# Performance work log

Hardware: AMD Instinct MI355X
Metric: run time of the kernel (lower is better)

## Reference

```python
import jax, jax.numpy as jnp
import numpy as np

N, D = 8192, 128
NUM_CLASSES = 512
LA, UA, K, S, LAMBDA_G, MARGIN = 10.0, 110.0, 3.0, 30.0, 1.0, 0.0


def setup_inputs() -> dict:
    key = jax.random.key(0)
    k1, k2, k3 = jax.random.split(key, 3)
    feat = jax.random.normal(k1, (N, D), dtype=jnp.float32)
    uc = jax.random.uniform(k2, (N,), dtype=jnp.float32)
    label = jax.random.randint(k3, (N,), 0, NUM_CLASSES, dtype=jnp.int64)
    return {"feat": feat, "uc": uc, "label": label}


def _safe_sqrt(d2):
    # matches torch cdist subgradient: grad 0 at exactly-zero distance
    pos = d2 > 0
    return jnp.where(pos, jnp.sqrt(jnp.where(pos, d2, 1.0)), 0.0)


def reference(feat, uc, label):
    # --- norm regularizer g (reg_type='exp_3') ---
    norms = jnp.linalg.norm(feat, axis=-1)                      # [N]
    nx = (norms - LA) / (UA - LA)
    ug = 2.7183 ** (-K)
    reg = ((jnp.exp(-nx * K) / K + ug * nx) / (1.0 - ug)).mean() * LAMBDA_G

    mask = label[:, None] == label[None, :]                      # [N, N] bool

    # normalize=True branch: unit-normalize then euclidean cdist
    f = feat / jnp.maximum(norms, 1e-12)[:, None]                # F.normalize
    gram = f @ f.T                                               # [N, N]
    d2 = jnp.clip(2.0 - 2.0 * gram, 0.0, None)
    similarity = -_safe_sqrt(d2)                                 # -cdist

    uc_pair = uc[:, None] + uc[None, :]
    correction = jnp.where(mask, -(uc_pair - MARGIN), uc_pair)

    similarity = jnp.arcsin(similarity / 2.0) * 2.0 - correction # convert_dist

    maskf = mask.astype(similarity.dtype)
    nmaskf = 1.0 - maskf
    s_pos = -similarity * maskf - 10.0 * nmaskf
    s_neg = similarity * nmaskf - 10.0 * maskf

    logit_p = jax.nn.logsumexp(s_pos * S, axis=-1)               # [N]
    logit_n = jax.nn.logsumexp(s_neg * S, axis=-1)               # [N]
    loss = jax.nn.softplus(logit_p + logit_n).mean()

    # forward returns loss/s + (reg - reg.detach()) (value == loss/s)
    out = loss / S + (reg - jax.lax.stop_gradient(reg))
    return out
```

## Files before the change

kernel.cpp:

```cpp
#include <hip/hip_runtime.h>
#include <hip/hip_bf16.h>
#include <stdint.h>

#define N_ROWS 8192
#define DIM 128
#define NCHUNK 16
#define CHUNK 512
#define JT 32
#define ROUNDS (CHUNK / JT)

#define S2D 43.2808512266689
#define PI2D 1.5707963267948966
#define CN 56.0f
#define CP 16.0f

typedef __attribute__((ext_vector_type(8))) short bf16x8;
typedef __attribute__((ext_vector_type(4))) float f32x4;


__device__ __forceinline__ unsigned short bf16_rne(float f) {
  uint32_t u = __float_as_uint(f);
  u += 0x7FFFu + ((u >> 16) & 1u);
  return (unsigned short)(u >> 16);
}
__device__ __forceinline__ float bf16_f(unsigned short h) {
  return __uint_as_float(((uint32_t)h) << 16);
}

__device__ __forceinline__ void gload16(const void* g, void* l) {
  __builtin_amdgcn_global_load_lds(
      (__attribute__((address_space(1))) void*)(void*)g,
      (__attribute__((address_space(3))) void*)l, 16, 0, 0);
}


__global__ __launch_bounds__(256) void prep_kernel(const float* __restrict__ feat,
                                                   unsigned short* __restrict__ fhi,
                                                   unsigned short* __restrict__ flo) {
  int w = threadIdx.x >> 6, l = threadIdx.x & 63;
  int row = blockIdx.x * 4 + w;
  float2 v = *(const float2*)(feat + (size_t)row * DIM + l * 2);
  float ss = v.x * v.x + v.y * v.y;
  #pragma unroll
  for (int m = 32; m; m >>= 1) ss += __shfl_xor(ss, m);
  float norm = sqrtf(ss);
  float scale = 1.0f / fmaxf(norm, 1e-12f);
  float fx = v.x * scale, fy = v.y * scale;
  unsigned short hx = bf16_rne(fx), hy = bf16_rne(fy);
  unsigned short lx = bf16_rne(fx - bf16_f(hx)), ly = bf16_rne(fy - bf16_f(hy));
  *(ushort2*)(fhi + (size_t)row * DIM + l * 2) = make_ushort2(hx, hy);
  *(ushort2*)(flo + (size_t)row * DIM + l * 2) = make_ushort2(lx, ly);
}


__global__ __launch_bounds__(256, 5) void pair_kernel(const unsigned short* __restrict__ fhi,
                                                      const unsigned short* __restrict__ flo,
                                                      const float* __restrict__ uc,
                                                      const int* __restrict__ label,
                                                      float2* __restrict__ partial) {
  __shared__ __attribute__((aligned(16))) char smem[2 * 16384];
  constexpr float S2 = (float)S2D;
  constexpr float S2PI2 = (float)(S2D * PI2D);
  constexpr float A0 = (float)(1.0 * S2D);
  constexpr float A1 = (float)(1.0 / 6.0 * S2D);
  constexpr float A2 = (float)(3.0 / 40.0 * S2D);
  constexpr float A3 = (float)(15.0 / 336.0 * S2D);
  constexpr float A4 = (float)(105.0 / 3456.0 * S2D);
  constexpr float A5 = (float)(945.0 / 42240.0 * S2D);

  const int t = threadIdx.x;
  const int w = t >> 6, l = t & 63;
  const int lr = l & 15, lg = l >> 4;
  const int i0 = blockIdx.x * 64;
  const int chunk = blockIdx.y;
  const char* fhb = (const char*)fhi;
  const char* flb = (const char*)flo;

  bf16x8 a_hi[4], a_lo[4];
  {
    int arow = i0 + w * 16 + lr;
    #pragma unroll
    for (int kk = 0; kk < 4; ++kk) {
      int off = arow * 256 + kk * 64 + lg * 16;
      a_hi[kk] = *(const bf16x8*)(fhb + off);
      a_lo[kk] = *(const bf16x8*)(flb + off);
    }
  }

  int li[4]; float uciS2[4];
  #pragma unroll
  for (int q = 0; q < 4; ++q) {
    int r = i0 + w * 16 + lg * 4 + q;
    li[q] = label[r];
    uciS2[q] = uc[r] * S2;
  }

  float sn[4] = {0.f, 0.f, 0.f, 0.f};
  float sp[4] = {0.f, 0.f, 0.f, 0.f};

  const int sw = (lr & 7) << 4;
  const int bb = lr * 256 + ((lg * 16) ^ (sw & 0x30));
  int koff[4];
  #pragma unroll
  for (int kk = 0; kk < 4; ++kk) koff[kk] = (kk * 64) ^ (sw & 0x40);

  int rc[2];
  #pragma unroll
  for (int c = 0; c < 2; ++c) {
    int aoff = c * 4096 + t * 16;
    int row = aoff >> 8;
    int off = aoff & 255;
    rc[c] = row * 256 + (off ^ ((row & 7) << 4));
  }
  const int ldst = w * 1024;

  size_t goff = (size_t)chunk * CHUNK * 256;

  #pragma unroll
  for (int c = 0; c < 2; ++c) {
    gload16(fhb + goff + rc[c], smem + c * 4096 + ldst);
    gload16(flb + goff + rc[c], smem + 8192 + c * 4096 + ldst);
  }
  __syncthreads();

  int cur = 0;
  for (int r = 0; r < ROUNDS; ++r) {
    const int j0 = chunk * CHUNK + r * JT;
    int lj_r[2]; float bn2[2], bp2[2];
    #pragma unroll
    for (int sub = 0; sub < 2; ++sub) {
      int j = j0 + sub * 16 + lr;
      lj_r[sub] = label[j];
      float uj = uc[j];
      bn2[sub] = fmaf(uj, S2, S2PI2 - CN);
      bp2[sub] = fmaf(uj, S2, CP - S2PI2);
    }
    if (r + 1 < ROUNDS) {
      const char* nb = smem + (cur ^ 1) * 16384;
      size_t g2 = goff + JT * 256;
      #pragma unroll
      for (int c = 0; c < 2; ++c) {
        gload16(fhb + g2 + rc[c], (void*)(nb + c * 4096 + ldst));
        gload16(flb + g2 + rc[c], (void*)(nb + 8192 + c * 4096 + ldst));
      }
    }

    const char* cb = smem + cur * 16384;
    #pragma unroll
    for (int sub = 0; sub < 2; ++sub) {
      f32x4 aA = {0.f,0.f,0.f,0.f}, aB = {0.f,0.f,0.f,0.f}, aC = {0.f,0.f,0.f,0.f};
      #pragma unroll
      for (int kk = 0; kk < 4; ++kk) {
        const char* ba = cb + bb + koff[kk] + sub * 4096;
        bf16x8 bh = *(const bf16x8*)(ba);
        bf16x8 bl = *(const bf16x8*)(ba + 8192);
        aA = __builtin_amdgcn_mfma_f32_16x16x32_bf16(a_hi[kk], bh, aA, 0, 0, 0);
        aB = __builtin_amdgcn_mfma_f32_16x16x32_bf16(a_hi[kk], bl, aB, 0, 0, 0);
        aC = __builtin_amdgcn_mfma_f32_16x16x32_bf16(a_lo[kk], bh, aC, 0, 0, 0);
      }
      f32x4 acc = aA + aB + aC;

      const int lj = lj_r[sub];
      const float bn = bn2[sub], bp = bp2[sub];
      #pragma unroll
      for (int q = 0; q < 4; ++q) {
        float g = acc[q];
        float u = g * g;
        float p = fmaf(u, A5, A4);
        p = fmaf(u, p, A3);
        p = fmaf(u, p, A2);
        p = fmaf(u, p, A1);
        p = fmaf(u, p, A0);
        float xp_ = g * p;
        bool same = (li[q] == lj);
        float vn = xp_ - (uciS2[q] + bn);
        vn = same ? -1e30f : vn;
        sn[q] += __builtin_amdgcn_exp2f(vn);
        if (same) {
          float vp = -(xp_ + uciS2[q] + bp);
          sp[q] += __builtin_amdgcn_exp2f(vp);
        }
      }
    }
    __syncthreads();
    goff += JT * 256;
    cur ^= 1;
  }

  #pragma unroll
  for (int q = 0; q < 4; ++q) {
    #pragma unroll
    for (int msk = 1; msk < 16; msk <<= 1) {
      sp[q] += __shfl_xor(sp[q], msk);
      sn[q] += __shfl_xor(sn[q], msk);
    }
  }
  if (lr == 0) {
    #pragma unroll
    for (int q = 0; q < 4; ++q) {
      int r = i0 + w * 16 + lg * 4 + q;
      partial[(size_t)r * NCHUNK + chunk] = make_float2(sp[q], sn[q]);
    }
  }
}


__global__ __launch_bounds__(256) void finalize1_kernel(const float2* __restrict__ partial,
                                                        float* __restrict__ blocksum) {
  int row = blockIdx.x * 256 + threadIdx.x;
  const float2* p = partial + (size_t)row * NCHUNK;
  float sp = 0.f, sn = 0.f;
  #pragma unroll
  for (int c = 0; c < NCHUNK; ++c) { float2 v = p[c]; sp += v.x; sn += v.y; }
  float z2 = log2f(sp) + log2f(sn) + (CP - CN);
  float z = 0.69314718056f * z2;
  float v = (z > 20.f) ? z : log1pf(__expf(z));
  #pragma unroll
  for (int m = 32; m; m >>= 1) v += __shfl_xor(v, m);
  __shared__ float ws4[4];
  if ((threadIdx.x & 63) == 0) ws4[threadIdx.x >> 6] = v;
  __syncthreads();
  if (threadIdx.x == 0) blocksum[blockIdx.x] = ws4[0] + ws4[1] + ws4[2] + ws4[3];
}


__global__ __launch_bounds__(64) void finalize2_kernel(const float* __restrict__ blocksum,
                                                       float* __restrict__ out) {
  int t = threadIdx.x;
  float v = (t < 32) ? blocksum[t] : 0.f;
  #pragma unroll
  for (int m = 32; m; m >>= 1) v += __shfl_xor(v, m);
  if (t == 0) out[0] = v * (1.0f / (8192.0f * 30.0f));
}


extern "C" void kernel_launch(void* const* d_in, const int* in_sizes, int n_in,
                              void* d_out, int out_size, void* d_ws, size_t ws_size,
                              hipStream_t stream) {
  const float* feat = (const float*)d_in[0];
  const float* uc   = (const float*)d_in[1];
  const int*   label = (const int*)d_in[2];
  float* out = (float*)d_out;
  char* ws = (char*)d_ws;

  unsigned short* fhi = (unsigned short*)ws;
  unsigned short* flo = (unsigned short*)(ws + (size_t)N_ROWS * DIM * 2);
  float2* partial = (float2*)(ws + (size_t)N_ROWS * DIM * 4);
  float* blocksum = (float*)(ws + (size_t)N_ROWS * DIM * 4
                             + (size_t)N_ROWS * NCHUNK * sizeof(float2));

  prep_kernel<<<N_ROWS / 4, 256, 0, stream>>>(feat, fhi, flo);
  pair_kernel<<<dim3(N_ROWS / 64, NCHUNK), 256, 0, stream>>>(fhi, flo, uc, label, partial);
  finalize1_kernel<<<N_ROWS / 256, 256, 0, stream>>>(partial, blocksum);
  finalize2_kernel<<<1, 64, 0, stream>>>(blocksum, out);
}
```

Measured before the change: 145.6 us.

## Compute positive-pair terms sparsely via class buckets; drop them from dense loop

Builds per-class index lists (counting sort in block 0 of the prep kernel) and moves the same-label positive-pair logsumexp out of the dense pair kernel into a finalize kernel. That kernel visits only same-class partners and uses a polynomial acos. The dense loop now accumulates only the negative sum and chains two MFMAs into one accumulator, which cuts an accumulator and the per-element branch. The two finalize kernels are merged into one that uses an atomic add into a zeroed output. The risks are a serial block-0 histogram inside prep and a different accuracy path for the positive terms.

```diff
diff --git a/kernel.cpp b/kernel.cpp
--- a/kernel.cpp
+++ b/kernel.cpp
@@ -4,6 +4,7 @@
 
 #define N_ROWS 8192
 #define DIM 128
+#define NCLS 512
 #define NCHUNK 16
 #define CHUNK 512
 #define JT 32
@@ -27,6 +28,19 @@
   return __uint_as_float(((uint32_t)h) << 16);
 }
 
+__device__ __forceinline__ float acos_fast(float x) {
+  float ax = fabsf(x);
+  float p = fmaf(ax, -0.0012624911f, 0.0066700901f);
+  p = fmaf(ax, p, -0.0170881256f);
+  p = fmaf(ax, p, 0.0308918810f);
+  p = fmaf(ax, p, -0.0501743046f);
+  p = fmaf(ax, p, 0.0889789874f);
+  p = fmaf(ax, p, -0.2145988016f);
+  p = fmaf(ax, p, 1.5707963050f);
+  float r = sqrtf(1.0f - ax) * p;
+  return x >= 0.0f ? r : 3.14159265358979f - r;
+}
+
 __device__ __forceinline__ void gload16(const void* g, void* l) {
   __builtin_amdgcn_global_load_lds(
       (__attribute__((address_space(1))) void*)(void*)g,
@@ -35,21 +49,60 @@
 
 
 __global__ __launch_bounds__(256) void prep_kernel(const float* __restrict__ feat,
+                                                   const int* __restrict__ label,
                                                    unsigned short* __restrict__ fhi,
-                                                   unsigned short* __restrict__ flo) {
-  int w = threadIdx.x >> 6, l = threadIdx.x & 63;
+                                                   unsigned short* __restrict__ flo,
+                                                   int* __restrict__ cls_start,
+                                                   int* __restrict__ cls_idx) {
+  __shared__ int cnt[NCLS];
+  __shared__ int ofs[NCLS];
+  const int t = threadIdx.x;
+  const int w = t >> 6, l = t & 63;
+
   int row = blockIdx.x * 4 + w;
   float2 v = *(const float2*)(feat + (size_t)row * DIM + l * 2);
   float ss = v.x * v.x + v.y * v.y;
   #pragma unroll
   for (int m = 32; m; m >>= 1) ss += __shfl_xor(ss, m);
-  float norm = sqrtf(ss);
-  float scale = 1.0f / fmaxf(norm, 1e-12f);
+  float scale = 1.0f / fmaxf(sqrtf(ss), 1e-12f);
   float fx = v.x * scale, fy = v.y * scale;
   unsigned short hx = bf16_rne(fx), hy = bf16_rne(fy);
   unsigned short lx = bf16_rne(fx - bf16_f(hx)), ly = bf16_rne(fy - bf16_f(hy));
   *(ushort2*)(fhi + (size_t)row * DIM + l * 2) = make_ushort2(hx, hy);
   *(ushort2*)(flo + (size_t)row * DIM + l * 2) = make_ushort2(lx, ly);
+
+  if (blockIdx.x == 0) {
+    for (int i = t; i < NCLS; i += 256) cnt[i] = 0;
+    __syncthreads();
+    for (int i = t; i < N_ROWS; i += 256) atomicAdd(&cnt[label[i]], 1);
+    __syncthreads();
+    if (t < 64) {
+      int loc[8];
+      int base = 0;
+      #pragma unroll
+      for (int b = 0; b < 8; ++b) { loc[b] = base; base += cnt[l * 8 + b]; }
+      int v2 = base;
+      #pragma unroll
+      for (int off = 1; off < 64; off <<= 1) {
+        int n = __shfl_up(v2, off);
+        if (l >= off) v2 += n;
+      }
+      int ex = v2 - base;
+      #pragma unroll
+      for (int b = 0; b < 8; ++b) {
+        int s = ex + loc[b];
+        ofs[l * 8 + b] = s;
+        cls_start[l * 8 + b] = s;
+      }
+      if (l == 63) cls_start[NCLS] = ex + base;
+    }
+    __syncthreads();
+    for (int i = t; i < N_ROWS; i += 256) {
+      int c = label[i];
+      int p = atomicAdd(&ofs[c], 1);
+      cls_idx[p] = i;
+    }
+  }
 }
 
 
@@ -57,7 +110,7 @@
                                                       const unsigned short* __restrict__ flo,
                                                       const float* __restrict__ uc,
                                                       const int* __restrict__ label,
-                                                      float2* __restrict__ partial) {
+                                                      float* __restrict__ partial) {
   __shared__ __attribute__((aligned(16))) char smem[2 * 16384];
   constexpr float S2 = (float)S2D;
   constexpr float S2PI2 = (float)(S2D * PI2D);
@@ -87,16 +140,15 @@
     }
   }
 
-  int li[4]; float uciS2[4];
+  int li[4]; float K0[4];
   #pragma unroll
   for (int q = 0; q < 4; ++q) {
     int r = i0 + w * 16 + lg * 4 + q;
     li[q] = label[r];
-    uciS2[q] = uc[r] * S2;
+    K0[q] = CN - S2PI2 - uc[r] * S2;
   }
 
   float sn[4] = {0.f, 0.f, 0.f, 0.f};
-  float sp[4] = {0.f, 0.f, 0.f, 0.f};
 
   const int sw = (lr & 7) << 4;
   const int bb = lr * 256 + ((lg * 16) ^ (sw & 0x30));
@@ -126,14 +178,12 @@
   int cur = 0;
   for (int r = 0; r < ROUNDS; ++r) {
     const int j0 = chunk * CHUNK + r * JT;
-    int lj_r[2]; float bn2[2], bp2[2];
+    int lj_r[2]; float us_r[2];
     #pragma unroll
     for (int sub = 0; sub < 2; ++sub) {
       int j = j0 + sub * 16 + lr;
       lj_r[sub] = label[j];
-      float uj = uc[j];
-      bn2[sub] = fmaf(uj, S2, S2PI2 - CN);
-      bp2[sub] = fmaf(uj, S2, CP - S2PI2);
+      us_r[sub] = uc[j] * S2;
     }
     if (r + 1 < ROUNDS) {
       const char* nb = smem + (cur ^ 1) * 16384;
@@ -145,23 +195,23 @@
       }
     }
 
-    const char* cb = smem + cur * 16384;
+    const char* cb_ = smem + cur * 16384;
     #pragma unroll
     for (int sub = 0; sub < 2; ++sub) {
-      f32x4 aA = {0.f,0.f,0.f,0.f}, aB = {0.f,0.f,0.f,0.f}, aC = {0.f,0.f,0.f,0.f};
+      f32x4 aA = {0.f,0.f,0.f,0.f}, aB = {0.f,0.f,0.f,0.f};
       #pragma unroll
       for (int kk = 0; kk < 4; ++kk) {
-        const char* ba = cb + bb + koff[kk] + sub * 4096;
+        const char* ba = cb_ + bb + koff[kk] + sub * 4096;
         bf16x8 bh = *(const bf16x8*)(ba);
         bf16x8 bl = *(const bf16x8*)(ba + 8192);
         aA = __builtin_amdgcn_mfma_f32_16x16x32_bf16(a_hi[kk], bh, aA, 0, 0, 0);
         aB = __builtin_amdgcn_mfma_f32_16x16x32_bf16(a_hi[kk], bl, aB, 0, 0, 0);
-        aC = __builtin_amdgcn_mfma_f32_16x16x32_bf16(a_lo[kk], bh, aC, 0, 0, 0);
-      }
-      f32x4 acc = aA + aB + aC;
+        aB = __builtin_amdgcn_mfma_f32_16x16x32_bf16(a_lo[kk], bh, aB, 0, 0, 0);
+      }
+      f32x4 acc = aA + aB;
 
       const int lj = lj_r[sub];
-      const float bn = bn2[sub], bp = bp2[sub];
+      const float us = us_r[sub];
       #pragma unroll
       for (int q = 0; q < 4; ++q) {
         float g = acc[q];
@@ -171,15 +221,9 @@
         p = fmaf(u, p, A2);
         p = fmaf(u, p, A1);
         p = fmaf(u, p, A0);
-        float xp_ = g * p;
-        bool same = (li[q] == lj);
-        float vn = xp_ - (uciS2[q] + bn);
-        vn = same ? -1e30f : vn;
+        float vn = fmaf(g, p, K0[q] - us);
+        vn = (li[q] == lj) ? -1e30f : vn;
         sn[q] += __builtin_amdgcn_exp2f(vn);
-        if (same) {
-          float vp = -(xp_ + uciS2[q] + bp);
-          sp[q] += __builtin_amdgcn_exp2f(vp);
-        }
       }
     }
     __syncthreads();
@@ -190,47 +234,68 @@
   #pragma unroll
   for (int q = 0; q < 4; ++q) {
     #pragma unroll
-    for (int msk = 1; msk < 16; msk <<= 1) {
-      sp[q] += __shfl_xor(sp[q], msk);
-      sn[q] += __shfl_xor(sn[q], msk);
-    }
+    for (int msk = 1; msk < 16; msk <<= 1) sn[q] += __shfl_xor(sn[q], msk);
   }
   if (lr == 0) {
     #pragma unroll
     for (int q = 0; q < 4; ++q) {
       int r = i0 + w * 16 + lg * 4 + q;
-      partial[(size_t)r * NCHUNK + chunk] = make_float2(sp[q], sn[q]);
-    }
-  }
-}
-
-
-__global__ __launch_bounds__(256) void finalize1_kernel(const float2* __restrict__ partial,
-                                                        float* __restrict__ blocksum) {
-  int row = blockIdx.x * 256 + threadIdx.x;
-  const float2* p = partial + (size_t)row * NCHUNK;
-  float sp = 0.f, sn = 0.f;
-  #pragma unroll
-  for (int c = 0; c < NCHUNK; ++c) { float2 v = p[c]; sp += v.x; sn += v.y; }
+      partial[(size_t)r * NCHUNK + chunk] = sn[q];
+    }
+  }
+}
+
+
+__global__ __launch_bounds__(256) void finalize_kernel(const unsigned short* __restrict__ fhi,
+                                                       const unsigned short* __restrict__ flo,
+                                                       const float* __restrict__ uc,
+                                                       const int* __restrict__ label,
+                                                       const float* __restrict__ partial,
+                                                       const int* __restrict__ cls_start,
+                                                       const int* __restrict__ cls_idx,
+                                                       float* __restrict__ out) {
+  constexpr float S2 = (float)S2D;
+  __shared__ float wsum[4];
+  const int t = threadIdx.x;
+  const int w = t >> 6, l = t & 63;
+  const int row = blockIdx.x * 4 + w;
+
+  float sn = (l < NCHUNK) ? partial[(size_t)row * NCHUNK + l] : 0.f;
+  #pragma unroll
+  for (int m = 32; m; m >>= 1) sn += __shfl_xor(sn, m);
+
+  ushort2 hi2 = *(const ushort2*)(fhi + (size_t)row * DIM + l * 2);
+  ushort2 lo2 = *(const ushort2*)(flo + (size_t)row * DIM + l * 2);
+  float fx = bf16_f(hi2.x) + bf16_f(lo2.x);
+  float fy = bf16_f(hi2.y) + bf16_f(lo2.y);
+
+  const int c = label[row];
+  const int ks = cls_start[c], ke = cls_start[c + 1];
+  const float uci = uc[row];
+  float sp = 0.f;
+  for (int k = ks; k < ke; ++k) {
+    int j = cls_idx[k];
+    ushort2 hj = *(const ushort2*)(fhi + (size_t)j * DIM + l * 2);
+    ushort2 lj = *(const ushort2*)(flo + (size_t)j * DIM + l * 2);
+    float g = fx * (bf16_f(hj.x) + bf16_f(lj.x)) + fy * (bf16_f(hj.y) + bf16_f(lj.y));
+    #pragma unroll
+    for (int m = 32; m; m >>= 1) g += __shfl_xor(g, m);
+    g = fminf(1.0f, fmaxf(-1.0f, g));
+    float th = acos_fast(g);
+    float vp = fmaf(S2, th, -S2 * (uci + uc[j]) - CP);
+    sp += __builtin_amdgcn_exp2f(vp);
+  }
+
   float z2 = log2f(sp) + log2f(sn) + (CP - CN);
   float z = 0.69314718056f * z2;
   float v = (z > 20.f) ? z : log1pf(__expf(z));
-  #pragma unroll
-  for (int m = 32; m; m >>= 1) v += __shfl_xor(v, m);
-  __shared__ float ws4[4];
-  if ((threadIdx.x & 63) == 0) ws4[threadIdx.x >> 6] = v;
+
+  if (l == 0) wsum[w] = v;
   __syncthreads();
-  if (threadIdx.x == 0) blocksum[blockIdx.x] = ws4[0] + ws4[1] + ws4[2] + ws4[3];
-}
-
-
-__global__ __launch_bounds__(64) void finalize2_kernel(const float* __restrict__ blocksum,
-                                                       float* __restrict__ out) {
-  int t = threadIdx.x;
-  float v = (t < 32) ? blocksum[t] : 0.f;
-  #pragma unroll
-  for (int m = 32; m; m >>= 1) v += __shfl_xor(v, m);
-  if (t == 0) out[0] = v * (1.0f / (8192.0f * 30.0f));
+  if (t == 0) {
+    float s = wsum[0] + wsum[1] + wsum[2] + wsum[3];
+    atomicAdd(out, s * (1.0f / (8192.0f * 30.0f)));
+  }
 }
 
 
@@ -245,12 +310,14 @@
 
   unsigned short* fhi = (unsigned short*)ws;
   unsigned short* flo = (unsigned short*)(ws + (size_t)N_ROWS * DIM * 2);
-  float2* partial = (float2*)(ws + (size_t)N_ROWS * DIM * 4);
-  float* blocksum = (float*)(ws + (size_t)N_ROWS * DIM * 4
-                             + (size_t)N_ROWS * NCHUNK * sizeof(float2));
-
-  prep_kernel<<<N_ROWS / 4, 256, 0, stream>>>(feat, fhi, flo);
+  float* partial = (float*)(ws + (size_t)N_ROWS * DIM * 4);
+  char* p2 = ws + (size_t)N_ROWS * DIM * 4 + (size_t)N_ROWS * NCHUNK * 4;
+  int* cls_start = (int*)p2;
+  int* cls_idx = (int*)(p2 + 2048 + 64);
+
+  hipMemsetAsync(out, 0, sizeof(float), stream);
+  prep_kernel<<<N_ROWS / 4, 256, 0, stream>>>(feat, label, fhi, flo, cls_start, cls_idx);
   pair_kernel<<<dim3(N_ROWS / 64, NCHUNK), 256, 0, stream>>>(fhi, flo, uc, label, partial);
-  finalize1_kernel<<<N_ROWS / 256, 256, 0, stream>>>(partial, blocksum);
-  finalize2_kernel<<<1, 64, 0, stream>>>(blocksum, out);
-}
+  finalize_kernel<<<N_ROWS / 4, 256, 0, stream>>>(fhi, flo, uc, label, partial,
+                                                  cls_start, cls_idx, out);
+}
```

Measured after the change: 183.0 us. +25.6%, slower.
